# Kernel optimization log

Measured on AMD Instinct MI355X. Metric: run time of the kernel, lower is better.

The kernel has to match this reference:

```python
import jax, jax.numpy as jnp
import numpy as np

SEQ_LEN = 512
VOCAB = 32000
EMB = 512
HID = 1024
NUM_CLASSES = 32000
BATCH = 64


def _lstm_layer(x, w_ih, w_hh, b_ih, b_hh):
    # x: [B, T, D_in]; PyTorch gate order i, f, g, o; weights [4H, D]
    B = x.shape[0]
    H = w_hh.shape[1]
    # precompute input projections for all timesteps: [T, B, 4H]
    xg = jnp.einsum('btd,gd->tbg', x, w_ih) + (b_ih + b_hh)

    def step(carry, xt):
        h, c = carry
        gates = xt + h @ w_hh.T  # [B, 4H]
        i, f, g, o = jnp.split(gates, 4, axis=-1)
        i = jax.nn.sigmoid(i)
        f = jax.nn.sigmoid(f)
        g = jnp.tanh(g)
        o = jax.nn.sigmoid(o)
        c = f * c + i * g
        h = o * jnp.tanh(c)
        return (h, c), h

    h0 = jnp.zeros((B, H), dtype=x.dtype)
    c0 = jnp.zeros((B, H), dtype=x.dtype)
    _, hs = jax.lax.scan(step, (h0, c0), xg)  # hs: [T, B, H]
    return jnp.transpose(hs, (1, 0, 2))  # [B, T, H]


def setup_inputs() -> dict:
    key = jax.random.key(0)
    ks = jax.random.split(key, 12)
    s_e = 1.0 / np.sqrt(EMB)
    s_h = 1.0 / np.sqrt(HID)
    inp = {
        'features': jax.random.randint(ks[0], (BATCH, SEQ_LEN), 0, VOCAB, dtype=jnp.int64)
            if jax.config.jax_enable_x64 else jax.random.randint(ks[0], (BATCH, SEQ_LEN), 0, VOCAB, dtype=jnp.int32),
        'emb': jax.random.normal(ks[1], (VOCAB + 1, EMB), jnp.float32),
        'w_ih0': jax.random.uniform(ks[2], (4 * HID, EMB), jnp.float32, -s_h, s_h),
        'w_hh0': jax.random.uniform(ks[3], (4 * HID, HID), jnp.float32, -s_h, s_h),
        'b_ih0': jax.random.uniform(ks[4], (4 * HID,), jnp.float32, -s_h, s_h),
        'b_hh0': jax.random.uniform(ks[5], (4 * HID,), jnp.float32, -s_h, s_h),
        'w_ih1': jax.random.uniform(ks[6], (4 * HID, HID), jnp.float32, -s_h, s_h),
        'w_hh1': jax.random.uniform(ks[7], (4 * HID, HID), jnp.float32, -s_h, s_h),
        'b_ih1': jax.random.uniform(ks[8], (4 * HID,), jnp.float32, -s_h, s_h),
        'b_hh1': jax.random.uniform(ks[9], (4 * HID,), jnp.float32, -s_h, s_h),
        'fc_w': jax.random.uniform(ks[10], (NUM_CLASSES, HID), jnp.float32, -s_h, s_h),
        'fc_b': jax.random.uniform(ks[11], (NUM_CLASSES,), jnp.float32, -s_h, s_h),
    }
    return inp


def reference(features, emb, w_ih0, w_hh0, b_ih0, b_hh0,
              w_ih1, w_hh1, b_ih1, b_hh1, fc_w, fc_b):
    # seq_lens = sum(features != vocab_size - 1) - 1
    seq_lens = jnp.sum(features != (VOCAB - 1), axis=1) - 1  # [B]
    x = emb[features]  # [B, T, E]
    h1 = _lstm_layer(x, w_ih0, w_hh0, b_ih0, b_hh0)   # [B, T, H]
    h2 = _lstm_layer(h1, w_ih1, w_hh1, b_ih1, b_hh1)  # [B, T, H]
    # gather output at seq_lens per batch row
    last = jnp.take_along_axis(h2, seq_lens[:, None, None].astype(jnp.int32), axis=1)[:, 0]  # [B, H]
    # dropout_rate = 0.0 -> identity
    pred = last @ fc_w.T + fc_b  # [B, num_classes]
    return pred
```

## Files before the change

### kernel.cpp

```cpp
#include <hip/hip_runtime.h>

#define NWG   256
#define NTHR  512
#define TSEQ  512
#define HID   1024
#define NCLS  32000
#define KP1   2056
#define KP0   1544
#define RP    44
#define PROG0 256
#define PROG1 1024
#define FJBASE 1600
#define FJL2   1856
#define FJFLAG 1888
#define SPIN_GUARD 10000000u
#define SCAN_GUARD 1000000u
#define SATUR 0x7FFFFFFFu

typedef __attribute__((ext_vector_type(8))) short short8;
typedef __attribute__((ext_vector_type(4))) float floatx4;

struct AB { short8 a[4]; short8 b[2]; };

__device__ __forceinline__ unsigned short f2bf(float f) {
  union { float f; unsigned u; } c; c.f = f;
  unsigned r = c.u + 0x7fffu + ((c.u >> 16) & 1u);
  return (unsigned short)(r >> 16);
}
__device__ __forceinline__ float sigmoidf_(float x) {
  x = fminf(30.f, fmaxf(-30.f, x));
  return 1.f / (1.f + __expf(-x));
}
__device__ __forceinline__ float tanhf_(float x) {
  x = fminf(15.f, fmaxf(-15.f, x));
  float e = __expf(2.f * x);
  return (e - 1.f) / (e + 1.f);
}
__device__ __forceinline__ void st_u32_agent(unsigned* p, unsigned v) {
  __hip_atomic_store(p, v, __ATOMIC_RELAXED, __HIP_MEMORY_SCOPE_AGENT);
}
__device__ __forceinline__ unsigned ld_u32_agent(const unsigned* p) {
  return __hip_atomic_load(p, __ATOMIC_RELAXED, __HIP_MEMORY_SCOPE_AGENT);
}

__device__ __forceinline__ void mfma8(const AB& f, floatx4 (&acc)[4][2]) {
#pragma unroll
  for (int mt = 0; mt < 4; ++mt)
#pragma unroll
    for (int nt = 0; nt < 2; ++nt)
      acc[mt][nt] = __builtin_amdgcn_mfma_f32_16x16x32_bf16(f.a[mt], f.b[nt], acc[mt][nt], 0, 0, 0);
}

template <int NKT, int KPAD>
__device__ __forceinline__ void gemm_part(
    int kb, int keo, int lm,
    const unsigned short* const (&ab)[4],
    const unsigned short* wl, floatx4 (&acc)[4][2])
{
  AB f0, f1;
  auto ld = [&](AB& f, int kt) {
    const int off = kb + kt * 32 + keo;
#pragma unroll
    for (int nt = 0; nt < 2; ++nt)
      f.b[nt] = *reinterpret_cast<const short8*>(wl + (nt * 16 + lm) * KPAD + off);
#pragma unroll
    for (int mt = 0; mt < 4; ++mt)
      f.a[mt] = *reinterpret_cast<const short8*>(ab[mt] + off);
  };
  ld(f0, 0);
#pragma unroll
  for (int kt = 0; kt + 2 < NKT; kt += 2) {
    ld(f1, kt + 1);
    mfma8(f0, acc);
    ld(f0, kt + 2);
    mfma8(f1, acc);
  }
  ld(f1, NKT - 1);
  mfma8(f0, acc);
  mfma8(f1, acc);
}

__global__ void __launch_bounds__(NTHR, 1)
lstm_kernel(const int* __restrict__ feat,
            const float* __restrict__ emb,
            const float* __restrict__ wih0, const float* __restrict__ whh0,
            const float* __restrict__ bih0, const float* __restrict__ bhh0,
            const float* __restrict__ wih1, const float* __restrict__ whh1,
            const float* __restrict__ bih1, const float* __restrict__ bhh1,
            const float* __restrict__ fcw, const float* __restrict__ fcb,
            float* __restrict__ out,
            unsigned* __restrict__ bar)
{
  const int tid  = threadIdx.x;
  const int wg   = blockIdx.x;
  const int wave = tid >> 6;
  const int lane = tid & 63;
  const int quad = lane >> 4;
  const int lm   = lane & 15;
  const int keo  = quad * 8;

  unsigned short* sc   = (unsigned short*)out;
  unsigned short* h0   = sc;
  unsigned short* h1   = sc + 524288;
  unsigned short* lh   = sc + 655360;
  unsigned short* xbuf = sc + 720896;

  const int layer = (wg >= 128) ? 1 : 0;
  const int wl_id = wg & 127;
  const int jb = wl_id * 8;

  __shared__ unsigned short wlds[32 * KP1];
  __shared__ float red[4][32][RP];
  __shared__ int   sl[64];
  __shared__ unsigned sdone[2];

  if (tid < 2) sdone[tid] = 0;

  {
    const float* wih = layer ? wih1 : wih0;
    const float* whh = layer ? whh1 : whh0;
    const int KX   = layer ? 1024 : 512;
    const int KTOT = layer ? 2048 : 1536;
    const int KPAD = layer ? KP1 : KP0;
    for (int r = 0; r < 32; ++r) {
      const int gr = (r >> 3) * HID + jb + (r & 7);
      for (int e4 = tid; e4 < (KTOT >> 2); e4 += NTHR) {
        const int k = e4 * 4;
        float4 v = (k < KX) ? *(const float4*)(wih + (size_t)gr * KX + k)
                            : *(const float4*)(whh + (size_t)gr * 1024 + (k - KX));
        ushort4 u; u.x = f2bf(v.x); u.y = f2bf(v.y); u.z = f2bf(v.z); u.w = f2bf(v.w);
        *(ushort4*)(wlds + r * KPAD + k) = u;
      }
    }
    if (layer && tid < 64) {
      int cnt = 0;
      const int* fr = feat + tid * TSEQ;
      for (int k = 0; k < TSEQ; k += 4)
        cnt += (fr[k] != 31999) + (fr[k + 1] != 31999) +
               (fr[k + 2] != 31999) + (fr[k + 3] != 31999);
      int v = cnt - 1; if (v < 0) v = 0;
      sl[tid] = v;
    }
  }
  __syncthreads();

  float bsum[4];
  float cv[2] = {0.f, 0.f};
  int   slv[2] = {0, 0};
  const int jl_c = tid & 7;
  const int bl_c = tid >> 3;
  if (tid < 256) {
    const float* bih = layer ? bih1 : bih0;
    const float* bhh = layer ? bhh1 : bhh0;
    const int gj = jb + jl_c;
#pragma unroll
    for (int g = 0; g < 4; ++g) bsum[g] = bih[g * HID + gj] + bhh[g * HID + gj];
    if (layer) { slv[0] = sl[bl_c]; slv[1] = sl[32 + bl_c]; }
  }

  auto scan1 = [&](int base, unsigned need) -> unsigned {
    unsigned g = 0, a0, a1;
    bool dead = false;
    for (;;) {
      a0 = ld_u32_agent(&bar[base + lane * 4]);
      a1 = ld_u32_agent(&bar[base + (64 + lane) * 4]);
      if (__all(a0 >= need && a1 >= need)) break;
      __builtin_amdgcn_s_sleep(1);
      if (++g > SCAN_GUARD) { dead = true; break; }
    }
    if (dead) return SATUR;
    unsigned m = a0 < a1 ? a0 : a1;
#pragma unroll
    for (int off = 32; off; off >>= 1) {
      unsigned o = (unsigned)__shfl_xor((int)m, off, 64);
      m = o < m ? o : m;
    }
    return m;
  };
  auto scan2 = [&](int baseA, unsigned needA, int baseB, unsigned needB,
                   unsigned& minA, unsigned& minB) {
    unsigned g = 0, a0, a1, b0, b1;
    bool dead = false;
    for (;;) {
      a0 = ld_u32_agent(&bar[baseA + lane * 4]);
      a1 = ld_u32_agent(&bar[baseA + (64 + lane) * 4]);
      b0 = ld_u32_agent(&bar[baseB + lane * 4]);
      b1 = ld_u32_agent(&bar[baseB + (64 + lane) * 4]);
      if (__all(a0 >= needA && a1 >= needA && b0 >= needB && b1 >= needB)) break;
      __builtin_amdgcn_s_sleep(1);
      if (++g > SCAN_GUARD) { dead = true; break; }
    }
    if (dead) { minA = SATUR; minB = SATUR; return; }
    unsigned ma = a0 < a1 ? a0 : a1;
    unsigned mb = b0 < b1 ? b0 : b1;
#pragma unroll
    for (int off = 32; off; off >>= 1) {
      unsigned oa = (unsigned)__shfl_xor((int)ma, off, 64); ma = oa < ma ? oa : ma;
      unsigned ob = (unsigned)__shfl_xor((int)mb, off, 64); mb = ob < mb ? ob : mb;
    }
    minA = ma; minB = mb;
  };
  auto spin_ge = [&](int idx, unsigned need) {
    unsigned g = 0;
    while (ld_u32_agent(&bar[idx]) < need) {
      __builtin_amdgcn_s_sleep(1);
      if (++g > SPIN_GUARD) break;
    }
  };

  auto reduce_cell = [&](floatx4 (&acc)[4][2], unsigned short* hw, int t) {
#pragma unroll
    for (int h = 0; h < 2; ++h) {
      if (wave < 4) {
#pragma unroll
        for (int mi = 0; mi < 2; ++mi)
#pragma unroll
          for (int nt = 0; nt < 2; ++nt)
#pragma unroll
            for (int r = 0; r < 4; ++r)
              red[wave][mi * 16 + quad * 4 + r][nt * 16 + lm] = acc[2 * h + mi][nt][r];
      }
      __syncthreads();
      if (wave >= 4) {
#pragma unroll
        for (int mi = 0; mi < 2; ++mi)
#pragma unroll
          for (int nt = 0; nt < 2; ++nt)
#pragma unroll
            for (int r = 0; r < 4; ++r)
              red[wave - 4][mi * 16 + quad * 4 + r][nt * 16 + lm] += acc[2 * h + mi][nt][r];
      }
      __syncthreads();
      if (tid < 256) {
        const int b = h * 32 + bl_c;
        float g0 = bsum[0], g1 = bsum[1], g2 = bsum[2], g3 = bsum[3];
#pragma unroll
        for (int v = 0; v < 4; ++v) {
          g0 += red[v][bl_c][jl_c];
          g1 += red[v][bl_c][8 + jl_c];
          g2 += red[v][bl_c][16 + jl_c];
          g3 += red[v][bl_c][24 + jl_c];
        }
        const float ig = sigmoidf_(g0);
        const float fg = sigmoidf_(g1);
        const float gg = tanhf_(g2);
        const float og = sigmoidf_(g3);
        const float cn = fg * cv[h] + ig * gg;
        cv[h] = cn;
        const float hn = og * tanhf_(cn);
        unsigned my = f2bf(hn);
        unsigned ov = (unsigned)__shfl_xor((int)my, 1, 64);
        if ((tid & 1) == 0) {
          const unsigned packed = my | (ov << 16);
          st_u32_agent((unsigned*)(hw + b * HID + jb + jl_c), packed);
          if (layer && t == slv[h])
            st_u32_agent((unsigned*)(lh + b * HID + jb + jl_c), packed);
        }
      }
      if (h == 0) __syncthreads();
    }
  };

  auto finish_step = [&](int par, unsigned r, int pbase) {
    if (wave < 4) {
      __builtin_amdgcn_s_waitcnt(0);
      if (lane == 0)
        __hip_atomic_fetch_add(&sdone[par], 1u, __ATOMIC_RELAXED, __HIP_MEMORY_SCOPE_WORKGROUP);
    } else if (wave == 7 && lane == 0) {
      unsigned g = 0;
      while (__hip_atomic_load(&sdone[par], __ATOMIC_RELAXED, __HIP_MEMORY_SCOPE_WORKGROUP) < 4u)
        if (++g > SPIN_GUARD) break;
      __hip_atomic_store(&sdone[par], 0u, __ATOMIC_RELAXED, __HIP_MEMORY_SCOPE_WORKGROUP);
      st_u32_agent(&bar[pbase + wl_id * 4], r);
    }
  };

  if (!layer) {
    if (tid < 256) {
      const int b = wl_id >> 1;
      const int off = (wl_id & 1) * 256 + tid;
#pragma unroll
      for (int tt = 0; tt < 2; ++tt) {
        unsigned xv = f2bf(emb[(size_t)feat[b * TSEQ + tt] * 512 + off]);
        unsigned ov = (unsigned)__shfl_xor((int)xv, 1, 64);
        if ((tid & 1) == 0)
          st_u32_agent((unsigned*)(xbuf + tt * 32768 + b * 512 + off), xv | (ov << 16));
      }
    }
    __builtin_amdgcn_s_waitcnt(0);
    __syncthreads();
    if (wave == 7 && lane == 0) st_u32_agent(&bar[PROG0 + wl_id * 4], 1u);
    unsigned seenOwn = 1, seenRing = 0;
    if (wave == 0) {
      seenOwn = scan1(PROG0, 1u);
      __builtin_amdgcn_fence(__ATOMIC_ACQUIRE, "agent");
    }
    __syncthreads();

    for (int t = 0; t < TSEQ; ++t) {
      if (t + 2 < TSEQ && tid < 256) {
        const int b = wl_id >> 1;
        const int off = (wl_id & 1) * 256 + tid;
        unsigned xv = f2bf(emb[(size_t)feat[b * TSEQ + (t + 2)] * 512 + off]);
        unsigned ov = (unsigned)__shfl_xor((int)xv, 1, 64);
        if ((tid & 1) == 0)
          st_u32_agent((unsigned*)(xbuf + ((t + 2) & 3) * 32768 + b * 512 + off), xv | (ov << 16));
      }

      floatx4 acc[4][2];
#pragma unroll
      for (int mt = 0; mt < 4; ++mt)
#pragma unroll
        for (int nt = 0; nt < 2; ++nt)
          acc[mt][nt] = (floatx4){0.f, 0.f, 0.f, 0.f};

      {
        const unsigned short* ab[4];
        const unsigned short* xq = xbuf + (size_t)(t & 3) * 32768;
#pragma unroll
        for (int mt = 0; mt < 4; ++mt) ab[mt] = xq + (mt * 16 + lm) * 512;
        gemm_part<2, KP0>(wave * 64, keo, lm, ab, wlds, acc);
      }

      if (wave == 0) {
        const unsigned needO = (unsigned)(t + 1);
        const unsigned needR = (t >= 8) ? (unsigned)(t - 7) : 0u;
        if (seenOwn < needO || seenRing < needR) {
          scan2(PROG0, needO, PROG1, needR, seenOwn, seenRing);
          __builtin_amdgcn_fence(__ATOMIC_ACQUIRE, "agent");
        }
      }
      __syncthreads();

      {
        const unsigned short* hb[4];
        const unsigned short* h0r = h0 + (size_t)((t + 7) & 7) * 65536;
#pragma unroll
        for (int mt = 0; mt < 4; ++mt) hb[mt] = h0r + (mt * 16 + lm) * HID - 512;
        gemm_part<4, KP0>(512 + wave * 128, keo, lm, hb, wlds, acc);
      }

      reduce_cell(acc, h0 + (size_t)(t & 7) * 65536, t);
      finish_step(t & 1, (unsigned)(t + 2), PROG0);
    }
  } else {
    unsigned seenX = 0;
    unsigned seenOwn = 0;
    for (int t = 0; t < TSEQ; ++t) {
      const unsigned needX = (unsigned)(t + 2);
      if (seenX < needX) {
        seenX = scan1(PROG0, needX);
        __builtin_amdgcn_fence(__ATOMIC_ACQUIRE, "agent");
      }

      floatx4 acc[4][2];
#pragma unroll
      for (int mt = 0; mt < 4; ++mt)
#pragma unroll
        for (int nt = 0; nt < 2; ++nt)
          acc[mt][nt] = (floatx4){0.f, 0.f, 0.f, 0.f};

      {
        const unsigned short* ab[4];
        const unsigned short* h0r = h0 + (size_t)(t & 7) * 65536;
#pragma unroll
        for (int mt = 0; mt < 4; ++mt) ab[mt] = h0r + (mt * 16 + lm) * HID;
        gemm_part<4, KP1>(wave * 128, keo, lm, ab, wlds, acc);
      }

      if (wave == 0) {
        const unsigned needO = (unsigned)t;
        if (seenOwn < needO) {
          seenOwn = scan1(PROG1, needO);
          __builtin_amdgcn_fence(__ATOMIC_ACQUIRE, "agent");
        }
      }
      __syncthreads();

      {
        const unsigned short* hb[4];
        const unsigned short* h1r = h1 + (size_t)((t + 1) & 1) * 65536;
#pragma unroll
        for (int mt = 0; mt < 4; ++mt) hb[mt] = h1r + (mt * 16 + lm) * HID - 1024;
        gemm_part<4, KP1>(1024 + wave * 128, keo, lm, hb, wlds, acc);
      }

      reduce_cell(acc, h1 + (size_t)(t & 1) * 65536, t);
      finish_step(t & 1, (unsigned)(t + 1), PROG1);
    }
  }

  auto sync_all = [&](unsigned r) {
    __builtin_amdgcn_s_waitcnt(0);
    __syncthreads();
    if (tid == 0) {
      unsigned old = __hip_atomic_fetch_add(&bar[FJBASE + (wg & 7) * 32], 1u,
                                            __ATOMIC_RELAXED, __HIP_MEMORY_SCOPE_AGENT);
      if (old == r * 32u - 1u) {
        unsigned mo = __hip_atomic_fetch_add(&bar[FJL2], 1u,
                                             __ATOMIC_RELAXED, __HIP_MEMORY_SCOPE_AGENT);
        if (mo == r * 8u - 1u)
          __hip_atomic_store(&bar[FJFLAG], r, __ATOMIC_RELAXED, __HIP_MEMORY_SCOPE_AGENT);
      }
      spin_ge(FJFLAG, r);
      __builtin_amdgcn_fence(__ATOMIC_ACQUIRE, "agent");
    }
    __syncthreads();
  };

  sync_all(1);

  const int colbase = wg * 125;
  const int col  = colbase + wave * 16 + lm;
  const int colc = (col < NCLS) ? col : (NCLS - 1);
  floatx4 facc[4];
  {
    const unsigned short* ab[4];
#pragma unroll
    for (int mt = 0; mt < 4; ++mt) ab[mt] = lh + (mt * 16 + lm) * HID;
    const float* bb = fcw + (size_t)colc * HID;

#pragma unroll
    for (int mt = 0; mt < 4; ++mt) facc[mt] = (floatx4){0.f, 0.f, 0.f, 0.f};

    short8 a0[4], a1[4], b0, b1;
    auto ld = [&](short8 (&A)[4], short8& B, int kbase) {
      const int off = kbase + keo;
      float4 v0 = *(const float4*)(bb + off);
      float4 v1 = *(const float4*)(bb + off + 4);
      short8 bv;
      bv[0] = (short)f2bf(v0.x); bv[1] = (short)f2bf(v0.y);
      bv[2] = (short)f2bf(v0.z); bv[3] = (short)f2bf(v0.w);
      bv[4] = (short)f2bf(v1.x); bv[5] = (short)f2bf(v1.y);
      bv[6] = (short)f2bf(v1.z); bv[7] = (short)f2bf(v1.w);
      B = bv;
#pragma unroll
      for (int mt = 0; mt < 4; ++mt)
        A[mt] = *reinterpret_cast<const short8*>(ab[mt] + off);
    };
    ld(a0, b0, 0);
#pragma unroll
    for (int kt = 0; kt < 30; kt += 2) {
      ld(a1, b1, (kt + 1) * 32);
#pragma unroll
      for (int mt = 0; mt < 4; ++mt)
        facc[mt] = __builtin_amdgcn_mfma_f32_16x16x32_bf16(a0[mt], b0, facc[mt], 0, 0, 0);
      ld(a0, b0, (kt + 2) * 32);
#pragma unroll
      for (int mt = 0; mt < 4; ++mt)
        facc[mt] = __builtin_amdgcn_mfma_f32_16x16x32_bf16(a1[mt], b1, facc[mt], 0, 0, 0);
    }
    ld(a1, b1, 31 * 32);
#pragma unroll
    for (int mt = 0; mt < 4; ++mt)
      facc[mt] = __builtin_amdgcn_mfma_f32_16x16x32_bf16(a0[mt], b0, facc[mt], 0, 0, 0);
#pragma unroll
    for (int mt = 0; mt < 4; ++mt)
      facc[mt] = __builtin_amdgcn_mfma_f32_16x16x32_bf16(a1[mt], b1, facc[mt], 0, 0, 0);
  }

  sync_all(2);

  if (col < colbase + 125) {
    const float bias = fcb[col];
#pragma unroll
    for (int mt = 0; mt < 4; ++mt)
#pragma unroll
      for (int r = 0; r < 4; ++r) {
        const int row = mt * 16 + quad * 4 + r;
        out[(size_t)row * NCLS + col] = facc[mt][r] + bias;
      }
  }
}

extern "C" void kernel_launch(void* const* d_in, const int* in_sizes, int n_in,
                              void* d_out, int out_size, void* d_ws, size_t ws_size,
                              hipStream_t stream) {
  (void)in_sizes; (void)n_in; (void)out_size; (void)ws_size;
  const int*   feat = (const int*)d_in[0];
  const float* emb  = (const float*)d_in[1];
  const float* wih0 = (const float*)d_in[2];
  const float* whh0 = (const float*)d_in[3];
  const float* bih0 = (const float*)d_in[4];
  const float* bhh0 = (const float*)d_in[5];
  const float* wih1 = (const float*)d_in[6];
  const float* whh1 = (const float*)d_in[7];
  const float* bih1 = (const float*)d_in[8];
  const float* bhh1 = (const float*)d_in[9];
  const float* fcw  = (const float*)d_in[10];
  const float* fcb  = (const float*)d_in[11];
  float*       out  = (float*)d_out;
  unsigned*    bar  = (unsigned*)d_ws;

  hipMemsetAsync(d_out, 0, 1703936, stream);
  hipMemsetAsync(d_ws, 0, 8192, stream);

  void* args[] = { &feat, &emb, &wih0, &whh0, &bih0, &bhh0, &wih1, &whh1,
                   &bih1, &bhh1, &fcw, &fcb, &out, &bar };
  hipLaunchCooperativeKernel((const void*)lstm_kernel, dim3(NWG), dim3(NTHR),
                             args, 0, stream);
}
```

Baseline: 5.842 ms.

## Load recurrent state with cache-bypassing loads and drop acquire fences

Replaces the double-buffered load/MFMA pipeline with a version that issues every activation load up front as inline-asm global_load_dwordx4 with sc0 sc1 bits. It then waits on vmcnt(0) once and runs all MFMAs back to back. Because these loads bypass the non-coherent caches, the agent-scope acquire fences after each spin-wait scan are removed. The aim is to take cache invalidation and fence cost off the per-timestep critical path. In exchange the MFMAs no longer overlap with loads, register pressure goes up, and correctness now depends on the sc bits giving coherent reads across workgroups.

```diff
diff --git a/kernel.cpp b/kernel.cpp
--- a/kernel.cpp
+++ b/kernel.cpp
@@ -20,8 +20,6 @@
 typedef __attribute__((ext_vector_type(8))) short short8;
 typedef __attribute__((ext_vector_type(4))) float floatx4;
 
-struct AB { short8 a[4]; short8 b[2]; };
-
 __device__ __forceinline__ unsigned short f2bf(float f) {
   union { float f; unsigned u; } c; c.f = f;
   unsigned r = c.u + 0x7fffu + ((c.u >> 16) & 1u);
@@ -43,41 +41,46 @@
   return __hip_atomic_load(p, __ATOMIC_RELAXED, __HIP_MEMORY_SCOPE_AGENT);
 }
 
-__device__ __forceinline__ void mfma8(const AB& f, floatx4 (&acc)[4][2]) {
-#pragma unroll
-  for (int mt = 0; mt < 4; ++mt)
-#pragma unroll
-    for (int nt = 0; nt < 2; ++nt)
-      acc[mt][nt] = __builtin_amdgcn_mfma_f32_16x16x32_bf16(f.a[mt], f.b[nt], acc[mt][nt], 0, 0, 0);
+__device__ __forceinline__ void ld16_sc(short8& d, const unsigned short* p, int kt) {
+  switch (kt) {
+  case 0:  asm volatile("global_load_dwordx4 %0, %1, off sc0 sc1"            : "=v"(d) : "v"(p)); break;
+  case 1:  asm volatile("global_load_dwordx4 %0, %1, off offset:64 sc0 sc1"  : "=v"(d) : "v"(p)); break;
+  case 2:  asm volatile("global_load_dwordx4 %0, %1, off offset:128 sc0 sc1" : "=v"(d) : "v"(p)); break;
+  default: asm volatile("global_load_dwordx4 %0, %1, off offset:192 sc0 sc1" : "=v"(d) : "v"(p)); break;
+  }
 }
 
 template <int NKT, int KPAD>
-__device__ __forceinline__ void gemm_part(
+__device__ __forceinline__ void gemm_sc(
     int kb, int keo, int lm,
     const unsigned short* const (&ab)[4],
     const unsigned short* wl, floatx4 (&acc)[4][2])
 {
-  AB f0, f1;
-  auto ld = [&](AB& f, int kt) {
+  short8 A[NKT][4];
+#pragma unroll
+  for (int mt = 0; mt < 4; ++mt) {
+    const unsigned short* p = ab[mt] + kb + keo;
+#pragma unroll
+    for (int kt = 0; kt < NKT; ++kt)
+      ld16_sc(A[kt][mt], p, kt);
+  }
+  short8 B[NKT][2];
+#pragma unroll
+  for (int kt = 0; kt < NKT; ++kt) {
     const int off = kb + kt * 32 + keo;
 #pragma unroll
     for (int nt = 0; nt < 2; ++nt)
-      f.b[nt] = *reinterpret_cast<const short8*>(wl + (nt * 16 + lm) * KPAD + off);
+      B[kt][nt] = *reinterpret_cast<const short8*>(wl + (nt * 16 + lm) * KPAD + off);
+  }
+  asm volatile("s_waitcnt vmcnt(0)" ::: "memory");
+  __builtin_amdgcn_sched_barrier(0);
+#pragma unroll
+  for (int kt = 0; kt < NKT; ++kt)
 #pragma unroll
     for (int mt = 0; mt < 4; ++mt)
-      f.a[mt] = *reinterpret_cast<const short8*>(ab[mt] + off);
-  };
-  ld(f0, 0);
-#pragma unroll
-  for (int kt = 0; kt + 2 < NKT; kt += 2) {
-    ld(f1, kt + 1);
-    mfma8(f0, acc);
-    ld(f0, kt + 2);
-    mfma8(f1, acc);
-  }
-  ld(f1, NKT - 1);
-  mfma8(f0, acc);
-  mfma8(f1, acc);
+#pragma unroll
+      for (int nt = 0; nt < 2; ++nt)
+        acc[mt][nt] = __builtin_amdgcn_mfma_f32_16x16x32_bf16(A[kt][mt], B[kt][nt], acc[mt][nt], 0, 0, 0);
 }
 
 __global__ void __launch_bounds__(NTHR, 1)
@@ -291,10 +294,7 @@
     __syncthreads();
     if (wave == 7 && lane == 0) st_u32_agent(&bar[PROG0 + wl_id * 4], 1u);
     unsigned seenOwn = 1, seenRing = 0;
-    if (wave == 0) {
-      seenOwn = scan1(PROG0, 1u);
-      __builtin_amdgcn_fence(__ATOMIC_ACQUIRE, "agent");
-    }
+    if (wave == 0) seenOwn = scan1(PROG0, 1u);
     __syncthreads();
 
     for (int t = 0; t < TSEQ; ++t) {
@@ -319,16 +319,14 @@
         const unsigned short* xq = xbuf + (size_t)(t & 3) * 32768;
 #pragma unroll
         for (int mt = 0; mt < 4; ++mt) ab[mt] = xq + (mt * 16 + lm) * 512;
-        gemm_part<2, KP0>(wave * 64, keo, lm, ab, wlds, acc);
+        gemm_sc<2, KP0>(wave * 64, keo, lm, ab, wlds, acc);
       }
 
       if (wave == 0) {
         const unsigned needO = (unsigned)(t + 1);
         const unsigned needR = (t >= 8) ? (unsigned)(t - 7) : 0u;
-        if (seenOwn < needO || seenRing < needR) {
+        if (seenOwn < needO || seenRing < needR)
           scan2(PROG0, needO, PROG1, needR, seenOwn, seenRing);
-          __builtin_amdgcn_fence(__ATOMIC_ACQUIRE, "agent");
-        }
       }
       __syncthreads();
 
@@ -337,7 +335,7 @@
         const unsigned short* h0r = h0 + (size_t)((t + 7) & 7) * 65536;
 #pragma unroll
         for (int mt = 0; mt < 4; ++mt) hb[mt] = h0r + (mt * 16 + lm) * HID - 512;
-        gemm_part<4, KP0>(512 + wave * 128, keo, lm, hb, wlds, acc);
+        gemm_sc<4, KP0>(512 + wave * 128, keo, lm, hb, wlds, acc);
       }
 
       reduce_cell(acc, h0 + (size_t)(t & 7) * 65536, t);
@@ -348,10 +346,7 @@
     unsigned seenOwn = 0;
     for (int t = 0; t < TSEQ; ++t) {
       const unsigned needX = (unsigned)(t + 2);
-      if (seenX < needX) {
-        seenX = scan1(PROG0, needX);
-        __builtin_amdgcn_fence(__ATOMIC_ACQUIRE, "agent");
-      }
+      if (seenX < needX) seenX = scan1(PROG0, needX);
 
       floatx4 acc[4][2];
 #pragma unroll
@@ -365,15 +360,12 @@
         const unsigned short* h0r = h0 + (size_t)(t & 7) * 65536;
 #pragma unroll
         for (int mt = 0; mt < 4; ++mt) ab[mt] = h0r + (mt * 16 + lm) * HID;
-        gemm_part<4, KP1>(wave * 128, keo, lm, ab, wlds, acc);
+        gemm_sc<4, KP1>(wave * 128, keo, lm, ab, wlds, acc);
       }
 
       if (wave == 0) {
         const unsigned needO = (unsigned)t;
-        if (seenOwn < needO) {
-          seenOwn = scan1(PROG1, needO);
-          __builtin_amdgcn_fence(__ATOMIC_ACQUIRE, "agent");
-        }
+        if (seenOwn < needO) seenOwn = scan1(PROG1, needO);
       }
       __syncthreads();
 
@@ -382,7 +374,7 @@
         const unsigned short* h1r = h1 + (size_t)((t + 1) & 1) * 65536;
 #pragma unroll
         for (int mt = 0; mt < 4; ++mt) hb[mt] = h1r + (mt * 16 + lm) * HID - 1024;
-        gemm_part<4, KP1>(1024 + wave * 128, keo, lm, hb, wlds, acc);
+        gemm_sc<4, KP1>(1024 + wave * 128, keo, lm, hb, wlds, acc);
       }
 
       reduce_cell(acc, h1 + (size_t)(t & 1) * 65536, t);
```

New measurement: 5.663 ms. 1.03x faster.
